# Optimization experiments

Hardware: AMD Instinct MI355X
Metric: run time of the kernel (lower is better)

The kernel has to match this reference:

```python
import jax, jax.numpy as jnp
import numpy as np

BN_EPS = 1e-3  # keras BatchNormalization default


def setup_inputs() -> dict:
    key = jax.random.key(0)
    ks = jax.random.split(key, 8)
    B, T, H, W, C = 2, 8, 28, 28, 256
    Ci = 128
    s_in = 1.0 / np.sqrt(C)
    s_ci = 1.0 / np.sqrt(Ci)
    return {
        "x": jax.random.normal(ks[0], (B, T, H, W, C), dtype=jnp.float32),
        "Wg": jax.random.normal(ks[1], (C, Ci), dtype=jnp.float32) * s_in,
        "bg": jnp.zeros((Ci,), dtype=jnp.float32),
        "Wt": jax.random.normal(ks[2], (C, Ci), dtype=jnp.float32) * s_in,
        "bt": jnp.zeros((Ci,), dtype=jnp.float32),
        "Wp": jax.random.normal(ks[3], (C, Ci), dtype=jnp.float32) * s_in,
        "bp": jnp.zeros((Ci,), dtype=jnp.float32),
        "Wo": jax.random.normal(ks[4], (Ci, C), dtype=jnp.float32) * s_ci,
        "bo": jnp.zeros((C,), dtype=jnp.float32),
        "gamma": jnp.ones((C,), dtype=jnp.float32),
        "beta": jnp.zeros((C,), dtype=jnp.float32),
        "moving_mean": jnp.zeros((C,), dtype=jnp.float32),
        "moving_var": jnp.ones((C,), dtype=jnp.float32),
    }


def reference(x, Wg, bg, Wt, bt, Wp, bp, Wo, bo, gamma, beta, moving_mean, moving_var):
    B, T, H, W, C = x.shape
    Ci = Wg.shape[1]
    N = T * H * W
    xf = x.reshape(B, N, C)  # flatten spatial-temporal positions
    # 1x1x1 convs are per-position channel GEMMs
    g_x = xf @ Wg + bg        # [B, N, Ci]
    theta_x = xf @ Wt + bt    # [B, N, Ci]
    phi_x = xf @ Wp + bp      # [B, N, Ci]
    # f = softmax(theta @ phi^T) -- unscaled single-head global attention
    f = jnp.einsum('bnc,bmc->bnm', theta_x, phi_x)  # [B, N, N]
    f = jax.nn.softmax(f, axis=-1)
    y = jnp.einsum('bnm,bmc->bnc', f, g_x)           # [B, N, Ci]
    # conv_out (1x1x1) back to C channels
    y = y @ Wo + bo                                   # [B, N, C]
    # BatchNorm, inference mode (training=None -> moving statistics)
    y = gamma * (y - moving_mean) * jax.lax.rsqrt(moving_var + BN_EPS) + beta
    return x + y.reshape(B, T, H, W, C)
```

## Files before the change

kernel.cpp:

```cpp
#include <hip/hip_runtime.h>

#define BB 2
#define NN 6272
#define CC 256
#define CI 128
#define SEG 7
#define KVSEG (NN / SEG)
#define LOG2E 1.44269504088896f
#define THR 12.0f

typedef _Float16 f16;
typedef __attribute__((ext_vector_type(2))) __fp16 fp16v2;
typedef __attribute__((ext_vector_type(8))) _Float16 f16x8;
typedef __attribute__((ext_vector_type(4))) float f32x4;

__global__ __launch_bounds__(256) void prep_kernel(
    const float* __restrict__ Wg, const float* __restrict__ Wt, const float* __restrict__ Wp,
    const float* __restrict__ Wo, const float* __restrict__ bg, const float* __restrict__ bt,
    const float* __restrict__ bp, const float* __restrict__ bo,
    const float* __restrict__ gamma, const float* __restrict__ beta,
    const float* __restrict__ mmean, const float* __restrict__ mvar,
    f16* __restrict__ WallT, f16* __restrict__ WoT,
    float* __restrict__ ball, float* __restrict__ bnsc, float* __restrict__ bnsh)
{
    const int idx = blockIdx.x * 256 + threadIdx.x;
    if (idx < 384*256) {
        const int j = idx >> 8, k = idx & 255;
        float v;
        if (j < 128)      v = Wg[k*CI + j];
        else if (j < 256) v = Wt[k*CI + (j-128)] * LOG2E;
        else              v = Wp[k*CI + (j-256)];
        WallT[j*256 + k] = (f16)v;
    } else if (idx < 384*256 + 256*128) {
        const int i2 = idx - 384*256;
        const int ci = i2 >> 7, k = i2 & 127;
        WoT[ci*CI + k] = (f16)Wo[k*CC + ci];
    } else {
        const int i3 = idx - (384*256 + 256*128);
        if (i3 < 384) {
            float v;
            if (i3 < 128)      v = bg[i3];
            else if (i3 < 256) v = bt[i3-128] * LOG2E;
            else               v = bp[i3-256];
            ball[i3] = v;
        } else if (i3 < 640) {
            const int c = i3 - 384;
            bnsc[c] = gamma[c] * rsqrtf(mvar[c] + 1e-3f);
        } else if (i3 < 896) {
            const int c = i3 - 640;
            float sc = gamma[c] * rsqrtf(mvar[c] + 1e-3f);
            bnsh[c] = beta[c] + sc * (bo[c] - mmean[c]);
        }
    }
}

__global__ __launch_bounds__(256) void proj_gemm(
    const float* __restrict__ x, const f16* __restrict__ WallT, const float* __restrict__ ball,
    f16* __restrict__ th, f16* __restrict__ ph, f16* __restrict__ gT)
{
    __shared__ __align__(16) f16 xls[16*264];
    __shared__ __align__(16) f16 gls[128*24];

    const int tid = threadIdx.x;
    const int wid = tid >> 6, lane = tid & 63;
    const int l15 = lane & 15, lg = lane >> 4;
    const int p0 = blockIdx.x * 16;
    const int nq = wid;

    {
        const int row = tid >> 4, seg = (tid & 15) * 16;
        const float* xsrc = x + (size_t)(p0 + row) * CC + seg;
        f16 buf[16];
        #pragma unroll
        for (int i = 0; i < 4; ++i) {
            float4 v = *reinterpret_cast<const float4*>(xsrc + 4*i);
            buf[4*i+0]=(f16)v.x; buf[4*i+1]=(f16)v.y; buf[4*i+2]=(f16)v.z; buf[4*i+3]=(f16)v.w;
        }
        *reinterpret_cast<f16x8*>(&xls[row*264 + seg])     = *reinterpret_cast<f16x8*>(&buf[0]);
        *reinterpret_cast<f16x8*>(&xls[row*264 + seg + 8]) = *reinterpret_cast<f16x8*>(&buf[8]);
    }
    __syncthreads();

    f32x4 acc[6];
    #pragma unroll
    for (int t = 0; t < 6; ++t) acc[t] = (f32x4){0.f,0.f,0.f,0.f};

    const f16* wbase = WallT + (size_t)(nq*96 + l15)*256 + lg*8;
    for (int kk = 0; kk < 8; ++kk) {
        f16x8 a = *reinterpret_cast<const f16x8*>(&xls[l15*264 + kk*32 + lg*8]);
        #pragma unroll
        for (int t = 0; t < 6; ++t) {
            f16x8 bfr = *reinterpret_cast<const f16x8*>(wbase + (size_t)t*16*256 + kk*32);
            acc[t] = __builtin_amdgcn_mfma_f32_16x16x32_f16(a, bfr, acc[t], 0, 0, 0);
        }
    }

    const int bidx = (p0 >= NN) ? 1 : 0;
    const int n0 = p0 - bidx * NN;
    const int prow = lg * 4;

    #pragma unroll
    for (int t = 0; t < 6; ++t) {
        const int j0 = nq*96 + t*16;
        const float bv = ball[j0 + l15];
        if (j0 < 128) {
            #pragma unroll
            for (int r = 0; r < 4; ++r)
                gls[(j0 + l15)*24 + prow + r] = (f16)(acc[t][r] + bv);
        } else if (j0 < 256) {
            f16* dst = th + (size_t)(p0 + prow)*CI + (j0 - 128) + l15;
            #pragma unroll
            for (int r = 0; r < 4; ++r)
                dst[(size_t)r*CI] = (f16)(acc[t][r] + bv);
        } else {
            f16* dst = ph + (size_t)(p0 + prow)*CI + (j0 - 256) + l15;
            #pragma unroll
            for (int r = 0; r < 4; ++r)
                dst[(size_t)r*CI] = (f16)(acc[t][r] + bv);
        }
    }
    __syncthreads();
    {
        const int ci = tid >> 1, part = tid & 1;
        f16x8 v = *reinterpret_cast<const f16x8*>(&gls[ci*24 + part*8]);
        f16* gdst = gT + ((size_t)bidx*CI + ci)*NN + n0 + part*8;
        *reinterpret_cast<f16x8*>(gdst) = v;
    }
}

__global__ __launch_bounds__(256, 3) void attn_kernel(
    const f16* __restrict__ th, const f16* __restrict__ ph,
    const f16* __restrict__ gT, float* __restrict__ pacc, float* __restrict__ pml)
{
    __shared__ __align__(16) f16 ph_lds[32 * 128];
    __shared__ __align__(16) f16 g_lds[128 * 32];
    __shared__ __align__(16) f16 pT_lds[4][2][16][40];

    const int b   = blockIdx.z;
    const int seg = blockIdx.y;
    const int tid = threadIdx.x;
    const int wid = tid >> 6;
    const int lane = tid & 63;
    const int l15 = lane & 15;
    const int lg  = lane >> 4;
    const int qw  = blockIdx.x * 128 + wid * 32;

    const f16* thb = th + (size_t)b * NN * CI;
    const f16* phb = ph + (size_t)b * NN * CI;
    const f16* gTb = gT + (size_t)b * CI * NN;

    f16x8 bf[2][4];
    #pragma unroll
    for (int qt = 0; qt < 2; ++qt) {
        const f16* trow = thb + (size_t)(qw + qt*16 + l15) * CI + lg * 8;
        #pragma unroll
        for (int kk = 0; kk < 4; ++kk)
            bf[qt][kk] = *reinterpret_cast<const f16x8*>(trow + kk * 32);
    }

    f32x4 acc[2][8];
    f32x4 accl[2];
    float m[2] = {-INFINITY, -INFINITY};
    #pragma unroll
    for (int qt = 0; qt < 2; ++qt) {
        #pragma unroll
        for (int ct = 0; ct < 8; ++ct) acc[qt][ct] = (f32x4){0.f,0.f,0.f,0.f};
        accl[qt] = (f32x4){0.f,0.f,0.f,0.f};
    }

    const f16x8 onesA = {(f16)1,(f16)1,(f16)1,(f16)1,(f16)1,(f16)1,(f16)1,(f16)1};

    const int prow = tid >> 3, pcol = (tid & 7) * 16;
    const int pswz = (prow & 7) << 3;
    const int growi = tid >> 1, gcol = (tid & 1) * 16;
    const int gswz = ((growi >> 1) & 3) << 3;
    const int gc0 = gcol ^ gswz, gc1 = (gcol + 8) ^ gswz;

    const int kv_base = seg * KVSEG;

    #pragma unroll 1
    for (int it = 0; it < KVSEG / 32; ++it) {
        const int kv0 = kv_base + it * 32;

        const f16* psrc = phb + (size_t)(kv0 + prow) * CI + pcol;
        const f16* gsrc = gTb + (size_t)growi * NN + kv0 + gcol;
        f16x8 pv0 = *reinterpret_cast<const f16x8*>(psrc);
        f16x8 pv1 = *reinterpret_cast<const f16x8*>(psrc + 8);
        f16x8 gv0 = *reinterpret_cast<const f16x8*>(gsrc);
        f16x8 gv1 = *reinterpret_cast<const f16x8*>(gsrc + 8);

        __syncthreads();
        *reinterpret_cast<f16x8*>(&ph_lds[prow*128 + (pcol ^ pswz)])       = pv0;
        *reinterpret_cast<f16x8*>(&ph_lds[prow*128 + ((pcol + 8) ^ pswz)]) = pv1;
        *reinterpret_cast<f16x8*>(&g_lds[growi*32 + gc0])                  = gv0;
        *reinterpret_cast<f16x8*>(&g_lds[growi*32 + gc1])                  = gv1;
        __syncthreads();

        f32x4 s00 = (f32x4){0.f,0.f,0.f,0.f}, s01 = (f32x4){0.f,0.f,0.f,0.f};
        f32x4 s10 = (f32x4){0.f,0.f,0.f,0.f}, s11 = (f32x4){0.f,0.f,0.f,0.f};
        const int xsw = (l15 & 7) << 3;
        #pragma unroll
        for (int kk = 0; kk < 4; ++kk) {
            const int coff = (kk*32 + lg*8) ^ xsw;
            f16x8 a0 = *reinterpret_cast<const f16x8*>(&ph_lds[l15*128 + coff]);
            f16x8 a1 = *reinterpret_cast<const f16x8*>(&ph_lds[(16 + l15)*128 + coff]);
            s00 = __builtin_amdgcn_mfma_f32_16x16x32_f16(a0, bf[0][kk], s00, 0, 0, 0);
            s01 = __builtin_amdgcn_mfma_f32_16x16x32_f16(a1, bf[0][kk], s01, 0, 0, 0);
            s10 = __builtin_amdgcn_mfma_f32_16x16x32_f16(a0, bf[1][kk], s10, 0, 0, 0);
            s11 = __builtin_amdgcn_mfma_f32_16x16x32_f16(a1, bf[1][kk], s11, 0, 0, 0);
        }

        float tm0 = fmaxf(fmaxf(fmaxf(s00[0], s00[1]), fmaxf(s00[2], s00[3])),
                          fmaxf(fmaxf(s01[0], s01[1]), fmaxf(s01[2], s01[3])));
        float tm1 = fmaxf(fmaxf(fmaxf(s10[0], s10[1]), fmaxf(s10[2], s10[3])),
                          fmaxf(fmaxf(s11[0], s11[1]), fmaxf(s11[2], s11[3])));
        tm0 = fmaxf(tm0, __shfl_xor(tm0, 16));
        tm0 = fmaxf(tm0, __shfl_xor(tm0, 32));
        tm1 = fmaxf(tm1, __shfl_xor(tm1, 16));
        tm1 = fmaxf(tm1, __shfl_xor(tm1, 32));
        if (__any((tm0 > m[0] + THR) || (tm1 > m[1] + THR))) {
            float nm0 = fmaxf(m[0], tm0), nm1 = fmaxf(m[1], tm1);
            float sc0 = __builtin_amdgcn_exp2f(m[0] - nm0);
            float sc1 = __builtin_amdgcn_exp2f(m[1] - nm1);
            m[0] = nm0; m[1] = nm1;
            #pragma unroll
            for (int ct = 0; ct < 8; ++ct) {
                acc[0][ct][0] *= sc0; acc[0][ct][1] *= sc0; acc[0][ct][2] *= sc0; acc[0][ct][3] *= sc0;
                acc[1][ct][0] *= sc1; acc[1][ct][1] *= sc1; acc[1][ct][2] *= sc1; acc[1][ct][3] *= sc1;
            }
            accl[0][0] *= sc0; accl[0][1] *= sc0; accl[0][2] *= sc0; accl[0][3] *= sc0;
            accl[1][0] *= sc1; accl[1][1] *= sc1; accl[1][2] *= sc1; accl[1][3] *= sc1;
        }

        {
            union { fp16v2 h[2]; float2 f; } u0, u1;
            u0.h[0] = __builtin_amdgcn_cvt_pkrtz(__builtin_amdgcn_exp2f(s00[0] - m[0]),
                                                 __builtin_amdgcn_exp2f(s00[1] - m[0]));
            u0.h[1] = __builtin_amdgcn_cvt_pkrtz(__builtin_amdgcn_exp2f(s00[2] - m[0]),
                                                 __builtin_amdgcn_exp2f(s00[3] - m[0]));
            u1.h[0] = __builtin_amdgcn_cvt_pkrtz(__builtin_amdgcn_exp2f(s01[0] - m[0]),
                                                 __builtin_amdgcn_exp2f(s01[1] - m[0]));
            u1.h[1] = __builtin_amdgcn_cvt_pkrtz(__builtin_amdgcn_exp2f(s01[2] - m[0]),
                                                 __builtin_amdgcn_exp2f(s01[3] - m[0]));
            *reinterpret_cast<float2*>(&pT_lds[wid][0][l15][4*lg])      = u0.f;
            *reinterpret_cast<float2*>(&pT_lds[wid][0][l15][16 + 4*lg]) = u1.f;
            u0.h[0] = __builtin_amdgcn_cvt_pkrtz(__builtin_amdgcn_exp2f(s10[0] - m[1]),
                                                 __builtin_amdgcn_exp2f(s10[1] - m[1]));
            u0.h[1] = __builtin_amdgcn_cvt_pkrtz(__builtin_amdgcn_exp2f(s10[2] - m[1]),
                                                 __builtin_amdgcn_exp2f(s10[3] - m[1]));
            u1.h[0] = __builtin_amdgcn_cvt_pkrtz(__builtin_amdgcn_exp2f(s11[0] - m[1]),
                                                 __builtin_amdgcn_exp2f(s11[1] - m[1]));
            u1.h[1] = __builtin_amdgcn_cvt_pkrtz(__builtin_amdgcn_exp2f(s11[2] - m[1]),
                                                 __builtin_amdgcn_exp2f(s11[3] - m[1]));
            *reinterpret_cast<float2*>(&pT_lds[wid][1][l15][4*lg])      = u0.f;
            *reinterpret_cast<float2*>(&pT_lds[wid][1][l15][16 + 4*lg]) = u1.f;
        }
        asm volatile("s_waitcnt lgkmcnt(0)" ::: "memory");
        f16x8 pa0 = *reinterpret_cast<const f16x8*>(&pT_lds[wid][0][l15][8*lg]);
        f16x8 pa1 = *reinterpret_cast<const f16x8*>(&pT_lds[wid][1][l15][8*lg]);

        const int grsw = ((l15 >> 1) & 3) << 3;
        #pragma unroll
        for (int ct = 0; ct < 8; ++ct) {
            f16x8 ga = *reinterpret_cast<const f16x8*>(&g_lds[(ct*16 + l15)*32 + (lg*8 ^ grsw)]);
            acc[0][ct] = __builtin_amdgcn_mfma_f32_16x16x32_f16(ga, pa0, acc[0][ct], 0, 0, 0);
            acc[1][ct] = __builtin_amdgcn_mfma_f32_16x16x32_f16(ga, pa1, acc[1][ct], 0, 0, 0);
        }
        accl[0] = __builtin_amdgcn_mfma_f32_16x16x32_f16(onesA, pa0, accl[0], 0, 0, 0);
        accl[1] = __builtin_amdgcn_mfma_f32_16x16x32_f16(onesA, pa1, accl[1], 0, 0, 0);
    }

    #pragma unroll
    for (int qt = 0; qt < 2; ++qt) {
        float* pb = pacc + (size_t)(b*SEG + seg) * CI * NN + qw + qt*16 + l15;
        #pragma unroll
        for (int ct = 0; ct < 8; ++ct)
            #pragma unroll
            for (int r = 0; r < 4; ++r)
                pb[(size_t)(ct*16 + lg*4 + r) * NN] = acc[qt][ct][r];
    }

    if (lg == 0) {
        #pragma unroll
        for (int qt = 0; qt < 2; ++qt) {
            float* mlb = pml + ((size_t)(b*SEG + seg) * NN + qw + qt*16 + l15) * 2;
            mlb[0] = m[qt];
            mlb[1] = accl[qt][0];
        }
    }
}

__global__ __launch_bounds__(256) void combine_kernel(
    const float* __restrict__ pacc, const float* __restrict__ pml,
    f16* __restrict__ yh)
{
    const int qL = threadIdx.x & 31;
    const int cg = threadIdx.x >> 5;
    const int q  = blockIdx.x * 32 + qL;
    const int b  = blockIdx.y;

    float mv[SEG], lv[SEG];
    #pragma unroll
    for (int s = 0; s < SEG; ++s) {
        const float* p = pml + ((size_t)(b*SEG + s) * NN + q) * 2;
        mv[s] = p[0];
        lv[s] = p[1];
    }
    float M = mv[0];
    #pragma unroll
    for (int s = 1; s < SEG; ++s) M = fmaxf(M, mv[s]);
    float wsum = 0.f, w[SEG];
    #pragma unroll
    for (int s = 0; s < SEG; ++s) {
        w[s] = __builtin_amdgcn_exp2f(mv[s] - M);
        wsum = fmaf(w[s], lv[s], wsum);
    }
    const float inv = 1.0f / wsum;

    const int c0 = cg * 16;
    float o[16];
    #pragma unroll
    for (int i = 0; i < 16; ++i) o[i] = 0.f;
    for (int s = 0; s < SEG; ++s) {
        const float* pb = pacc + ((size_t)(b*SEG + s) * CI + c0) * NN + q;
        #pragma unroll
        for (int i = 0; i < 16; ++i)
            o[i] = fmaf(w[s], pb[(size_t)i * NN], o[i]);
    }
    f16 oh[16];
    #pragma unroll
    for (int i = 0; i < 16; ++i) oh[i] = (f16)(o[i] * inv);
    f16* yo = yh + ((size_t)b * NN + q) * CI + c0;
    *reinterpret_cast<f16x8*>(yo)     = *reinterpret_cast<f16x8*>(&oh[0]);
    *reinterpret_cast<f16x8*>(yo + 8) = *reinterpret_cast<f16x8*>(&oh[8]);
}

__global__ __launch_bounds__(256) void out_gemm(
    const float* __restrict__ x, const f16* __restrict__ yh, const f16* __restrict__ WoT,
    const float* __restrict__ bnsc, const float* __restrict__ bnsh, float* __restrict__ out)
{
    const int tid = threadIdx.x;
    const int wid = tid >> 6, lane = tid & 63;
    const int l15 = lane & 15, lg = lane >> 4;
    const int p0 = blockIdx.x * 16;
    const int nq = wid;

    f32x4 acc[4];
    #pragma unroll
    for (int t = 0; t < 4; ++t) acc[t] = (f32x4){0.f,0.f,0.f,0.f};

    const f16* ya = yh + (size_t)(p0 + l15)*CI + lg*8;
    const f16* wb = WoT + (size_t)(nq*64 + l15)*CI + lg*8;
    #pragma unroll
    for (int kk = 0; kk < 4; ++kk) {
        f16x8 a = *reinterpret_cast<const f16x8*>(ya + kk*32);
        #pragma unroll
        for (int t = 0; t < 4; ++t) {
            f16x8 bfr = *reinterpret_cast<const f16x8*>(wb + (size_t)t*16*CI + kk*32);
            acc[t] = __builtin_amdgcn_mfma_f32_16x16x32_f16(a, bfr, acc[t], 0, 0, 0);
        }
    }

    #pragma unroll
    for (int t = 0; t < 4; ++t) {
        const int ci = nq*64 + t*16 + l15;
        const float sc = bnsc[ci], sh = bnsh[ci];
        #pragma unroll
        for (int r = 0; r < 4; ++r) {
            const size_t idx = (size_t)(p0 + lg*4 + r)*CC + ci;
            out[idx] = x[idx] + fmaf(sc, acc[t][r], sh);
        }
    }
}

extern "C" void kernel_launch(void* const* d_in, const int* in_sizes, int n_in,
                              void* d_out, int out_size, void* d_ws, size_t ws_size,
                              hipStream_t stream)
{
    const float* x     = (const float*)d_in[0];
    const float* Wg    = (const float*)d_in[1];
    const float* bg    = (const float*)d_in[2];
    const float* Wt    = (const float*)d_in[3];
    const float* bt    = (const float*)d_in[4];
    const float* Wp    = (const float*)d_in[5];
    const float* bp    = (const float*)d_in[6];
    const float* Wo    = (const float*)d_in[7];
    const float* bo    = (const float*)d_in[8];
    const float* gamma = (const float*)d_in[9];
    const float* beta  = (const float*)d_in[10];
    const float* mmean = (const float*)d_in[11];
    const float* mvar  = (const float*)d_in[12];
    float* out = (float*)d_out;

    const size_t PB = (size_t)BB * NN * CI;
    f16*   th   = (f16*)d_ws;
    f16*   ph   = th + PB;
    f16*   gT   = ph + PB;
    float* pacc = (float*)(gT + PB);
    float* pml  = pacc + (size_t)BB * SEG * NN * CI;
    f16*   yh   = (f16*)(pml + (size_t)BB * SEG * NN * 2);
    f16*   WallT= yh + PB;
    f16*   WoT  = WallT + 384*256;
    float* ball = (float*)(WoT + 256*CI);
    float* bnsc = ball + 384;
    float* bnsh = bnsc + 256;

    prep_kernel<<<516, 256, 0, stream>>>(Wg, Wt, Wp, Wo, bg, bt, bp, bo,
                                         gamma, beta, mmean, mvar,
                                         WallT, WoT, ball, bnsc, bnsh);
    proj_gemm<<<BB * NN / 16, 256, 0, stream>>>(x, WallT, ball, th, ph, gT);
    attn_kernel<<<dim3(NN / 128, SEG, BB), 256, 0, stream>>>(th, ph, gT, pacc, pml);
    combine_kernel<<<dim3(NN / 32, BB), 256, 0, stream>>>(pacc, pml, yh);
    out_gemm<<<BB * NN / 16, 256, 0, stream>>>(x, yh, WoT, bnsc, bnsh, out);
}
```

Before: 114.7 us.

## Double-buffer phi tiles in LDS and load g operands directly into registers

The attention loop now double-buffers the phi tile in shared memory. Each iteration prefetches the next tile's phi rows into registers and writes them to the alternate buffer after the PV MFMAs, so only one barrier per iteration remains. The g tile no longer goes through LDS: each wave loads its MFMA A-operands for g straight from global memory into registers, prefetched one iteration ahead. This removes one barrier and the g LDS staging. In exchange, each wave loads g redundantly from global memory and holds more registers, which could reduce occupancy under the 3-blocks launch bound.

```diff
diff --git a/kernel.cpp b/kernel.cpp
--- a/kernel.cpp
+++ b/kernel.cpp
@@ -6,6 +6,7 @@
 #define CI 128
 #define SEG 7
 #define KVSEG (NN / SEG)
+#define NIT (KVSEG / 32)
 #define LOG2E 1.44269504088896f
 #define THR 12.0f
 
@@ -132,8 +133,7 @@
     const f16* __restrict__ th, const f16* __restrict__ ph,
     const f16* __restrict__ gT, float* __restrict__ pacc, float* __restrict__ pml)
 {
-    __shared__ __align__(16) f16 ph_lds[32 * 128];
-    __shared__ __align__(16) f16 g_lds[128 * 32];
+    __shared__ __align__(16) f16 ph_lds[2][32 * 128];
     __shared__ __align__(16) f16 pT_lds[4][2][16][40];
 
     const int b   = blockIdx.z;
@@ -172,29 +172,36 @@
 
     const int prow = tid >> 3, pcol = (tid & 7) * 16;
     const int pswz = (prow & 7) << 3;
-    const int growi = tid >> 1, gcol = (tid & 1) * 16;
-    const int gswz = ((growi >> 1) & 3) << 3;
-    const int gc0 = gcol ^ gswz, gc1 = (gcol + 8) ^ gswz;
+    const int pc0 = pcol ^ pswz, pc1 = (pcol + 8) ^ pswz;
 
     const int kv_base = seg * KVSEG;
 
+    {
+        const f16* ps = phb + (size_t)(kv_base + prow) * CI + pcol;
+        f16x8 a = *reinterpret_cast<const f16x8*>(ps);
+        f16x8 c = *reinterpret_cast<const f16x8*>(ps + 8);
+        *reinterpret_cast<f16x8*>(&ph_lds[0][prow*128 + pc0]) = a;
+        *reinterpret_cast<f16x8*>(&ph_lds[0][prow*128 + pc1]) = c;
+    }
+    f16x8 ga[8];
+    #pragma unroll
+    for (int ct = 0; ct < 8; ++ct)
+        ga[ct] = *reinterpret_cast<const f16x8*>(gTb + (size_t)(ct*16 + l15)*NN + kv_base + lg*8);
+    __syncthreads();
+
     #pragma unroll 1
-    for (int it = 0; it < KVSEG / 32; ++it) {
+    for (int it = 0; it < NIT; ++it) {
         const int kv0 = kv_base + it * 32;
-
-        const f16* psrc = phb + (size_t)(kv0 + prow) * CI + pcol;
-        const f16* gsrc = gTb + (size_t)growi * NN + kv0 + gcol;
-        f16x8 pv0 = *reinterpret_cast<const f16x8*>(psrc);
-        f16x8 pv1 = *reinterpret_cast<const f16x8*>(psrc + 8);
-        f16x8 gv0 = *reinterpret_cast<const f16x8*>(gsrc);
-        f16x8 gv1 = *reinterpret_cast<const f16x8*>(gsrc + 8);
-
-        __syncthreads();
-        *reinterpret_cast<f16x8*>(&ph_lds[prow*128 + (pcol ^ pswz)])       = pv0;
-        *reinterpret_cast<f16x8*>(&ph_lds[prow*128 + ((pcol + 8) ^ pswz)]) = pv1;
-        *reinterpret_cast<f16x8*>(&g_lds[growi*32 + gc0])                  = gv0;
-        *reinterpret_cast<f16x8*>(&g_lds[growi*32 + gc1])                  = gv1;
-        __syncthreads();
+        const f16* cbuf = &ph_lds[it & 1][0];
+        f16* nbuf = &ph_lds[(it + 1) & 1][0];
+        const bool havenext = (it + 1 < NIT);
+
+        f16x8 pv0, pv1;
+        if (havenext) {
+            const f16* ps = phb + (size_t)(kv0 + 32 + prow) * CI + pcol;
+            pv0 = *reinterpret_cast<const f16x8*>(ps);
+            pv1 = *reinterpret_cast<const f16x8*>(ps + 8);
+        }
 
         f32x4 s00 = (f32x4){0.f,0.f,0.f,0.f}, s01 = (f32x4){0.f,0.f,0.f,0.f};
         f32x4 s10 = (f32x4){0.f,0.f,0.f,0.f}, s11 = (f32x4){0.f,0.f,0.f,0.f};
@@ -202,8 +209,8 @@
         #pragma unroll
         for (int kk = 0; kk < 4; ++kk) {
             const int coff = (kk*32 + lg*8) ^ xsw;
-            f16x8 a0 = *reinterpret_cast<const f16x8*>(&ph_lds[l15*128 + coff]);
-            f16x8 a1 = *reinterpret_cast<const f16x8*>(&ph_lds[(16 + l15)*128 + coff]);
+            f16x8 a0 = *reinterpret_cast<const f16x8*>(&cbuf[l15*128 + coff]);
+            f16x8 a1 = *reinterpret_cast<const f16x8*>(&cbuf[(16 + l15)*128 + coff]);
             s00 = __builtin_amdgcn_mfma_f32_16x16x32_f16(a0, bf[0][kk], s00, 0, 0, 0);
             s01 = __builtin_amdgcn_mfma_f32_16x16x32_f16(a1, bf[0][kk], s01, 0, 0, 0);
             s10 = __builtin_amdgcn_mfma_f32_16x16x32_f16(a0, bf[1][kk], s10, 0, 0, 0);
@@ -259,15 +266,23 @@
         f16x8 pa0 = *reinterpret_cast<const f16x8*>(&pT_lds[wid][0][l15][8*lg]);
         f16x8 pa1 = *reinterpret_cast<const f16x8*>(&pT_lds[wid][1][l15][8*lg]);
 
-        const int grsw = ((l15 >> 1) & 3) << 3;
         #pragma unroll
         for (int ct = 0; ct < 8; ++ct) {
-            f16x8 ga = *reinterpret_cast<const f16x8*>(&g_lds[(ct*16 + l15)*32 + (lg*8 ^ grsw)]);
-            acc[0][ct] = __builtin_amdgcn_mfma_f32_16x16x32_f16(ga, pa0, acc[0][ct], 0, 0, 0);
-            acc[1][ct] = __builtin_amdgcn_mfma_f32_16x16x32_f16(ga, pa1, acc[1][ct], 0, 0, 0);
+            acc[0][ct] = __builtin_amdgcn_mfma_f32_16x16x32_f16(ga[ct], pa0, acc[0][ct], 0, 0, 0);
+            acc[1][ct] = __builtin_amdgcn_mfma_f32_16x16x32_f16(ga[ct], pa1, acc[1][ct], 0, 0, 0);
         }
         accl[0] = __builtin_amdgcn_mfma_f32_16x16x32_f16(onesA, pa0, accl[0], 0, 0, 0);
         accl[1] = __builtin_amdgcn_mfma_f32_16x16x32_f16(onesA, pa1, accl[1], 0, 0, 0);
+
+        if (havenext) {
+            #pragma unroll
+            for (int ct = 0; ct < 8; ++ct)
+                ga[ct] = *reinterpret_cast<const f16x8*>(
+                    gTb + (size_t)(ct*16 + l15)*NN + kv0 + 32 + lg*8);
+            *reinterpret_cast<f16x8*>(&nbuf[prow*128 + pc0]) = pv0;
+            *reinterpret_cast<f16x8*>(&nbuf[prow*128 + pc1]) = pv1;
+        }
+        __syncthreads();
     }
 
     #pragma unroll
```

New measurement: 236.9 us. 2.07x slower.

## Double KV split count, tile gT layout, store normalized partials in fp16

Applied to the files above, without the earlier changes.

Doubles the number of KV segments in the split-KV attention so the grid has twice as many blocks and fills the GPU better. gT is stored in 32-position tiles so each block's G load is one contiguous chunk. Each segment's partial output is normalized by its own row sum and written as fp16, halving partial-buffer traffic, and the combine step reweights partials by exp(m-M)*l. More segments mean more partial writes and a longer combine pass, and the fp16 partials add a little rounding.

```diff
diff --git a/kernel.cpp b/kernel.cpp
--- a/kernel.cpp
+++ b/kernel.cpp
@@ -4,8 +4,9 @@
 #define NN 6272
 #define CC 256
 #define CI 128
-#define SEG 7
+#define SEG 14
 #define KVSEG (NN / SEG)
+#define NIT (KVSEG / 32)
 #define LOG2E 1.44269504088896f
 #define THR 12.0f
 
@@ -123,14 +124,15 @@
     {
         const int ci = tid >> 1, part = tid & 1;
         f16x8 v = *reinterpret_cast<const f16x8*>(&gls[ci*24 + part*8]);
-        f16* gdst = gT + ((size_t)bidx*CI + ci)*NN + n0 + part*8;
+        f16* gdst = gT + ((size_t)bidx*(NN/32) + (n0 >> 5))*(CI*32)
+                       + ci*32 + (n0 & 16) + part*8;
         *reinterpret_cast<f16x8*>(gdst) = v;
     }
 }
 
 __global__ __launch_bounds__(256, 3) void attn_kernel(
     const f16* __restrict__ th, const f16* __restrict__ ph,
-    const f16* __restrict__ gT, float* __restrict__ pacc, float* __restrict__ pml)
+    const f16* __restrict__ gT, f16* __restrict__ pacc, float* __restrict__ pml)
 {
     __shared__ __align__(16) f16 ph_lds[32 * 128];
     __shared__ __align__(16) f16 g_lds[128 * 32];
@@ -147,7 +149,7 @@
 
     const f16* thb = th + (size_t)b * NN * CI;
     const f16* phb = ph + (size_t)b * NN * CI;
-    const f16* gTb = gT + (size_t)b * CI * NN;
+    const f16* gTb = gT + (size_t)b * (NN/32) * (CI*32);
 
     f16x8 bf[2][4];
     #pragma unroll
@@ -172,33 +174,35 @@
 
     const int prow = tid >> 3, pcol = (tid & 7) * 16;
     const int pswz = (prow & 7) << 3;
-    const int growi = tid >> 1, gcol = (tid & 1) * 16;
-    const int gswz = ((growi >> 1) & 3) << 3;
-    const int gc0 = gcol ^ gswz, gc1 = (gcol + 8) ^ gswz;
+    const int pc0 = pcol ^ pswz, pc1 = (pcol + 8) ^ pswz;
+    const int grow = tid >> 1, gcs = (tid & 1) * 16;
+    const int gswz = ((grow >> 1) & 3) << 3;
+    const int gc0 = gcs ^ gswz, gc1 = (gcs + 8) ^ gswz;
 
     const int kv_base = seg * KVSEG;
+    const int t0 = kv_base >> 5;
+    const int xsw = (l15 & 7) << 3;
 
     #pragma unroll 1
-    for (int it = 0; it < KVSEG / 32; ++it) {
+    for (int it = 0; it < NIT; ++it) {
         const int kv0 = kv_base + it * 32;
 
-        const f16* psrc = phb + (size_t)(kv0 + prow) * CI + pcol;
-        const f16* gsrc = gTb + (size_t)growi * NN + kv0 + gcol;
-        f16x8 pv0 = *reinterpret_cast<const f16x8*>(psrc);
-        f16x8 pv1 = *reinterpret_cast<const f16x8*>(psrc + 8);
-        f16x8 gv0 = *reinterpret_cast<const f16x8*>(gsrc);
-        f16x8 gv1 = *reinterpret_cast<const f16x8*>(gsrc + 8);
+        const f16* ps = phb + (size_t)(kv0 + prow) * CI + pcol;
+        f16x8 pv0 = *reinterpret_cast<const f16x8*>(ps);
+        f16x8 pv1 = *reinterpret_cast<const f16x8*>(ps + 8);
+        const f16* gs = gTb + (size_t)(t0 + it) * (CI*32) + tid * 16;
+        f16x8 gv0 = *reinterpret_cast<const f16x8*>(gs);
+        f16x8 gv1 = *reinterpret_cast<const f16x8*>(gs + 8);
 
         __syncthreads();
-        *reinterpret_cast<f16x8*>(&ph_lds[prow*128 + (pcol ^ pswz)])       = pv0;
-        *reinterpret_cast<f16x8*>(&ph_lds[prow*128 + ((pcol + 8) ^ pswz)]) = pv1;
-        *reinterpret_cast<f16x8*>(&g_lds[growi*32 + gc0])                  = gv0;
-        *reinterpret_cast<f16x8*>(&g_lds[growi*32 + gc1])                  = gv1;
+        *reinterpret_cast<f16x8*>(&ph_lds[prow*128 + pc0]) = pv0;
+        *reinterpret_cast<f16x8*>(&ph_lds[prow*128 + pc1]) = pv1;
+        *reinterpret_cast<f16x8*>(&g_lds[grow*32 + gc0])   = gv0;
+        *reinterpret_cast<f16x8*>(&g_lds[grow*32 + gc1])   = gv1;
         __syncthreads();
 
         f32x4 s00 = (f32x4){0.f,0.f,0.f,0.f}, s01 = (f32x4){0.f,0.f,0.f,0.f};
         f32x4 s10 = (f32x4){0.f,0.f,0.f,0.f}, s11 = (f32x4){0.f,0.f,0.f,0.f};
-        const int xsw = (l15 & 7) << 3;
         #pragma unroll
         for (int kk = 0; kk < 4; ++kk) {
             const int coff = (kk*32 + lg*8) ^ xsw;
@@ -270,14 +274,15 @@
         accl[1] = __builtin_amdgcn_mfma_f32_16x16x32_f16(onesA, pa1, accl[1], 0, 0, 0);
     }
 
+    const float inv[2] = {1.0f / accl[0][0], 1.0f / accl[1][0]};
     #pragma unroll
     for (int qt = 0; qt < 2; ++qt) {
-        float* pb = pacc + (size_t)(b*SEG + seg) * CI * NN + qw + qt*16 + l15;
+        f16* pb = pacc + (size_t)(b*SEG + seg) * CI * NN + qw + qt*16 + l15;
         #pragma unroll
         for (int ct = 0; ct < 8; ++ct)
             #pragma unroll
             for (int r = 0; r < 4; ++r)
-                pb[(size_t)(ct*16 + lg*4 + r) * NN] = acc[qt][ct][r];
+                pb[(size_t)(ct*16 + lg*4 + r) * NN] = (f16)(acc[qt][ct][r] * inv[qt]);
     }
 
     if (lg == 0) {
@@ -291,7 +296,7 @@
 }
 
 __global__ __launch_bounds__(256) void combine_kernel(
-    const float* __restrict__ pacc, const float* __restrict__ pml,
+    const f16* __restrict__ pacc, const float* __restrict__ pml,
     f16* __restrict__ yh)
 {
     const int qL = threadIdx.x & 31;
@@ -309,11 +314,11 @@
     float M = mv[0];
     #pragma unroll
     for (int s = 1; s < SEG; ++s) M = fmaxf(M, mv[s]);
-    float wsum = 0.f, w[SEG];
+    float wsum = 0.f, wl[SEG];
     #pragma unroll
     for (int s = 0; s < SEG; ++s) {
-        w[s] = __builtin_amdgcn_exp2f(mv[s] - M);
-        wsum = fmaf(w[s], lv[s], wsum);
+        wl[s] = __builtin_amdgcn_exp2f(mv[s] - M) * lv[s];
+        wsum += wl[s];
     }
     const float inv = 1.0f / wsum;
 
@@ -322,10 +327,10 @@
     #pragma unroll
     for (int i = 0; i < 16; ++i) o[i] = 0.f;
     for (int s = 0; s < SEG; ++s) {
-        const float* pb = pacc + ((size_t)(b*SEG + s) * CI + c0) * NN + q;
+        const f16* pb = pacc + ((size_t)(b*SEG + s) * CI + c0) * NN + q;
         #pragma unroll
         for (int i = 0; i < 16; ++i)
-            o[i] = fmaf(w[s], pb[(size_t)i * NN], o[i]);
+            o[i] = fmaf(wl[s], (float)pb[(size_t)i * NN], o[i]);
     }
     f16 oh[16];
     #pragma unroll
@@ -396,8 +401,8 @@
     f16*   th   = (f16*)d_ws;
     f16*   ph   = th + PB;
     f16*   gT   = ph + PB;
-    float* pacc = (float*)(gT + PB);
-    float* pml  = pacc + (size_t)BB * SEG * NN * CI;
+    f16*   pacc = gT + PB;
+    float* pml  = (float*)(pacc + (size_t)BB * SEG * NN * CI);
     f16*   yh   = (f16*)(pml + (size_t)BB * SEG * NN * 2);
     f16*   WallT= yh + PB;
     f16*   WoT  = WallT + 384*256;
```

Result: slower. 122.8 us (+7.1%).
